# Optimization experiments

Measured on AMD Instinct MI355X. Metric: run time of the kernel, lower is better.

## Reference

```python
import jax, jax.numpy as jnp
import numpy as np

N_USER = 100000
N_ITEM = 100000
SUPP = 10000
B = 1024
L = 50
S = 256
H = 4
E = 64
HID = 64


def setup_inputs() -> dict:
    key = jax.random.key(0)
    ks = jax.random.split(key, 32)
    f32 = jnp.float32
    inp = {}
    # forward int args
    inp["x"] = jax.random.randint(ks[0], (B, 2), 0, N_USER)
    inp["src_his"] = jax.random.randint(ks[1], (B, L), 0, N_ITEM)
    inp["src_hl"] = jax.random.randint(ks[2], (B,), 0, L)
    inp["tgt_his"] = jax.random.randint(ks[3], (B, L), 0, N_ITEM)
    inp["tgt_hl"] = jax.random.randint(ks[4], (B,), 0, L)
    # precomputed neighbor sampling: [2 get_user_emb calls, H heads, B, S]
    inp["sample_idx"] = jax.random.randint(ks[5], (2, H, B, S), 0, SUPP)
    inp["supp_users"] = jax.random.randint(ks[6], (SUPP,), 0, N_USER)
    # embedding tables (xavier-ish small scale)
    inp["src_user_emb"] = jax.random.normal(ks[7], (N_USER, E), f32) * 0.1
    inp["src_item_emb"] = jax.random.normal(ks[8], (N_ITEM, E), f32) * 0.1
    inp["tgt_user_emb"] = jax.random.normal(ks[9], (N_USER, E), f32) * 0.1
    inp["tgt_item_emb"] = jax.random.normal(ks[10], (N_ITEM, E), f32) * 0.1
    # attention / aggregation weights, stored [in, out]
    s = 1.0 / np.sqrt(E)
    inp["W_att_w"] = jax.random.normal(ks[11], (E, E), f32) * s
    inp["W_att_b"] = jnp.full((E,), 0.1, f32)
    inp["W_agg_w"] = jax.random.normal(ks[12], (E, E), f32) * s
    # per-head GAT projections, batched over heads
    inp["Wq"] = jax.random.normal(ks[13], (H, E, E), f32) * s
    inp["Wk"] = jax.random.normal(ks[14], (H, E, E), f32) * s
    inp["Wv"] = jax.random.normal(ks[15], (H, E, E), f32) * s
    inp["W_out"] = jax.random.normal(ks[16], (H * E, E), f32) * (1.0 / np.sqrt(H * E))
    # scoring MLP
    inp["l1_w"] = jax.random.normal(ks[17], (2 * E, HID), f32) * (1.0 / np.sqrt(2 * E))
    inp["l1_b"] = jnp.full((HID,), 0.1, f32)
    inp["l2_w"] = jax.random.normal(ks[18], (HID, E), f32) * (1.0 / np.sqrt(HID))
    inp["l2_b"] = jnp.full((E,), 0.1, f32)
    inp["l3_w"] = jax.random.normal(ks[19], (E, 1), f32) * s
    inp["l3_b"] = jnp.full((1,), 0.1, f32)
    return inp


def reference(x, src_his, src_hl, tgt_his, tgt_hl, sample_idx, supp_users,
              src_user_emb, src_item_emb, tgt_user_emb, tgt_item_emb,
              W_att_w, W_att_b, W_agg_w, Wq, Wk, Wv, W_out,
              l1_w, l1_b, l2_w, l2_b, l3_w, l3_b):
    user_id = x[:, 0]
    item_id = x[:, 1]

    def user_fea_encode(his, hl, user_table):
        # NOTE: original always gathers from src_model.item_embedding (even for tgt)
        Lh = his.shape[1]
        valid = jnp.arange(Lh)[None, :] < hl[:, None]          # [B,L]
        hist = src_item_emb[his] * valid[..., None]             # [B,L,E], padded rows zeroed
        u = user_table[user_id]                                 # [B,E]
        keyt = jnp.tanh(hist @ W_att_w + W_att_b)               # [B,L,E]
        pad = hist.sum(-1) == 0                                 # [B,L]
        att = jnp.einsum('ble,be->bl', keyt, u)
        # faithful masked_softmax: masked scores set to 0 BEFORE exp (exp(0)=1 still contributes)
        att = jnp.where(pad, 0.0, att)
        e = jnp.exp(att)
        att = e / (jnp.sum(e, axis=1, keepdims=True) + 1e-12)
        out = jnp.einsum('bl,ble->be', att, hist)
        return out @ W_agg_w                                    # W_agg has no bias

    def get_user_emb(fea, idx):
        # idx: [H,B,S] indices into supp_users; all heads batched in one einsum chain
        neigh = tgt_user_emb[supp_users[idx]]                   # [H,B,S,E]
        q = jnp.einsum('be,heo->hbo', fea, Wq)                  # [H,B,O]
        k = jnp.einsum('hbse,heo->hbso', neigh, Wk)             # [H,B,S,O]
        attn = jax.nn.softmax(jnp.einsum('hbo,hbso->hbs', q, k), axis=-1)
        ctx = jnp.einsum('hbs,hbso->hbo', attn, k)              # weighted sum over neighbors
        g = jnp.einsum('hbo,hop->hbp', ctx, Wv)                 # [H,B,O]
        g = jnp.transpose(g, (1, 0, 2)).reshape(fea.shape[0], -1)  # concat heads -> [B,H*O]
        return g @ W_out

    user_src_fea = user_fea_encode(src_his, src_hl, src_user_emb)
    user_emb = get_user_emb(user_src_fea, sample_idx[0])
    item_emb = tgt_item_emb[item_id]
    user_tgt_fea = user_fea_encode(tgt_his, tgt_hl, tgt_user_emb)
    hybrid_tgt_emb = get_user_emb(user_tgt_fea, sample_idx[1])

    x_t = jnp.concatenate([hybrid_tgt_emb, item_emb], axis=1)
    x1_t = jnp.tanh(x_t @ l1_w + l1_b)
    x2_t = jnp.tanh(x1_t @ l2_w + l2_b)
    x3_t = (x2_t @ l3_w + l3_b).reshape(-1)

    output = jnp.sum(user_emb * item_emb, axis=1)
    out_emb_s = user_emb * item_emb
    # (output, output_t, out_emb_s, out_emb_t); train=False branch (sim/domain heads are None)
    return (output, x3_t, out_emb_s, x2_t)
```

## Files before the change

### kernel.cpp

```cpp
#include <hip/hip_runtime.h>

constexpr int B    = 1024;
constexpr int L    = 50;
constexpr int S    = 256;
constexpr int H    = 4;
constexpr int E    = 64;
constexpr int HID  = 64;
constexpr int SUPP = 10000;

__device__ __forceinline__ float lanebc(float v, int l) {
    return __int_as_float(__builtin_amdgcn_readlane(__float_as_int(v), l));
}

__global__ __launch_bounds__(256) void pre_kernel(
    const int* __restrict__ x,
    const int* __restrict__ src_his,
    const int* __restrict__ src_hl,
    const int* __restrict__ tgt_his,
    const int* __restrict__ tgt_hl,
    const float* __restrict__ item_emb,
    const float* __restrict__ src_user_emb,
    const float* __restrict__ tgt_user_emb,
    const int* __restrict__ supp_users,
    const float* __restrict__ W_att_w,
    const float* __restrict__ W_att_b,
    const float* __restrict__ W_agg_w,
    const float* __restrict__ Wq,
    const float* __restrict__ Wk,
    float* __restrict__ qout,
    float* __restrict__ K_supp)
{
    const int tid  = threadIdx.x;
    const int lane = tid & 63;
    const int wave = tid >> 6;

    if (blockIdx.y == 2) {
        const int h = wave;
        float wcol[E];
#pragma unroll
        for (int i = 0; i < E; i++) wcol[i] = Wk[h * E * E + i * E + lane];

#pragma unroll 2
        for (int j = blockIdx.x; j < SUPP; j += gridDim.x) {
            const int u = supp_users[j];
            const float ev = tgt_user_emb[(size_t)u * E + lane];
            float acc = 0.0f;
#pragma unroll
            for (int i = 0; i < E; i++) acc += lanebc(ev, i) * wcol[i];
            K_supp[((size_t)h * SUPP + j) * E + lane] = acc;
        }
        return;
    }

    __shared__ float sHist[L * E];
    __shared__ float sAtt[L];
    __shared__ float sPart[4][E];
    __shared__ float sOut[E];

    const int b    = blockIdx.x;
    const int call = blockIdx.y;

    const int* his = call ? tgt_his : src_his;
    const int* hl  = call ? tgt_hl  : src_hl;
    const float* user_table = call ? tgt_user_emb : src_user_emb;

    float wcol[E];
#pragma unroll
    for (int i = 0; i < E; i++) wcol[i] = W_att_w[i * E + lane];

    const int uid    = x[2 * b];
    const float uv   = user_table[(size_t)uid * E + lane];
    const float bias = W_att_b[lane];
    const int hlen   = hl[b];

    for (int l = wave; l < L; l += 4) {
        const int it = his[b * L + l];
        const float hv = (l < hlen) ? item_emb[(size_t)it * E + lane] : 0.0f;
        sHist[l * E + lane] = hv;
        float a = bias;
#pragma unroll
        for (int i = 0; i < E; i++) a += lanebc(hv, i) * wcol[i];
        float part = tanhf(a) * uv;
        float hsum = hv;
#pragma unroll
        for (int off = 32; off; off >>= 1) {
            part += __shfl_xor(part, off);
            hsum += __shfl_xor(hsum, off);
        }
        if (lane == 0) sAtt[l] = (hsum == 0.0f) ? 0.0f : part;
    }
    __syncthreads();

    if (wave == 0) {
        float v = (lane < L) ? expf(sAtt[lane]) : 0.0f;
        float s = v;
#pragma unroll
        for (int off = 32; off; off >>= 1) s += __shfl_xor(s, off);
        const float denom = s + 1e-12f;
        if (lane < L) sAtt[lane] = v / denom;
    }
    __syncthreads();

    float c = 0.0f;
    for (int l = wave; l < L; l += 4) c += sAtt[l] * sHist[l * E + lane];
    sPart[wave][lane] = c;
    __syncthreads();
    if (tid < E) sOut[tid] = sPart[0][tid] + sPart[1][tid] + sPart[2][tid] + sPart[3][tid];
    __syncthreads();

    float g = 0.0f;
#pragma unroll
    for (int k = 0; k < 16; k++) {
        const int i = wave * 16 + k;
        g += sOut[i] * W_agg_w[i * E + lane];
    }
    sPart[wave][lane] = g;
    __syncthreads();

    const float fval = sPart[0][lane] + sPart[1][lane] + sPart[2][lane] + sPart[3][lane];
    const float* Wqh = Wq + wave * E * E;
    float qacc = 0.0f;
#pragma unroll
    for (int i = 0; i < E; i++) qacc += lanebc(fval, i) * Wqh[i * E + lane];
    qout[(((call * H) + wave) * B + b) * E + lane] = qacc;
}

__global__ __launch_bounds__(256) void attn_kernel(
    const int* __restrict__ sample_idx,
    const float* __restrict__ K_supp,
    const float* __restrict__ qarr,
    const float* __restrict__ Wv,
    float* __restrict__ gout)
{
    __shared__ float sRed[8];
    __shared__ float sCtx[4][E];
    __shared__ float sC[E];
    __shared__ float sG[4][E];

    const int b    = blockIdx.x;
    const int h    = blockIdx.y;
    const int call = blockIdx.z;
    const int tid  = threadIdx.x;
    const int lane = tid & 63;
    const int wave = tid >> 6;
    const int u    = lane & 15;
    const int rsub = lane >> 4;
    const int s0   = wave * 64;

    const int* idx = sample_idx + (((call * H) + h) * B + b) * S;
    const float* Kh = K_supp + (size_t)h * SUPP * E;
    const float4 qu = *(const float4*)(qarr + ((size_t)(((call * H) + h) * B + b)) * E + 4 * u);

    float4 kreg[16];
    float mylogit = 0.0f;
#pragma unroll
    for (int i = 0; i < 16; i++) {
        const int j = idx[s0 + 4 * i + rsub];
        kreg[i] = *(const float4*)(Kh + (size_t)j * E + 4 * u);
        float part = kreg[i].x * qu.x + kreg[i].y * qu.y
                   + kreg[i].z * qu.z + kreg[i].w * qu.w;
#pragma unroll
        for (int off = 1; off < 16; off <<= 1) part += __shfl_xor(part, off);
        mylogit = (u == i) ? part : mylogit;
    }

    float m = mylogit;
#pragma unroll
    for (int off = 32; off; off >>= 1) m = fmaxf(m, __shfl_xor(m, off));
    if (lane == 0) sRed[wave] = m;
    __syncthreads();
    const float mx = fmaxf(fmaxf(sRed[0], sRed[1]), fmaxf(sRed[2], sRed[3]));
    const float ex = expf(mylogit - mx);
    float sm = ex;
#pragma unroll
    for (int off = 32; off; off >>= 1) sm += __shfl_xor(sm, off);
    if (lane == 0) sRed[4 + wave] = sm;
    __syncthreads();
    const float denom = sRed[4] + sRed[5] + sRed[6] + sRed[7];
    const float pval = ex / denom;

    float4 cacc = make_float4(0.0f, 0.0f, 0.0f, 0.0f);
#pragma unroll
    for (int i = 0; i < 16; i++) {
        const float p = __shfl(pval, (lane & 48) + i);
        cacc.x += p * kreg[i].x;
        cacc.y += p * kreg[i].y;
        cacc.z += p * kreg[i].z;
        cacc.w += p * kreg[i].w;
    }
#pragma unroll
    for (int off = 16; off <= 32; off <<= 1) {
        cacc.x += __shfl_xor(cacc.x, off);
        cacc.y += __shfl_xor(cacc.y, off);
        cacc.z += __shfl_xor(cacc.z, off);
        cacc.w += __shfl_xor(cacc.w, off);
    }
    if (lane < 16) *(float4*)(&sCtx[wave][u * 4]) = cacc;
    __syncthreads();
    if (wave == 0) {
        sC[lane] = sCtx[0][lane] + sCtx[1][lane] + sCtx[2][lane] + sCtx[3][lane];
    }
    __syncthreads();

    const float* Wvh = Wv + h * E * E;
    float g = 0.0f;
#pragma unroll
    for (int k = 0; k < 16; k++) {
        const int c = wave * 16 + k;
        g += sC[c] * Wvh[c * E + lane];
    }
    sG[wave][lane] = g;
    __syncthreads();
    if (wave == 0) {
        gout[((size_t)(call * B) + b) * (H * E) + h * E + lane] =
            sG[0][lane] + sG[1][lane] + sG[2][lane] + sG[3][lane];
    }
}

__global__ __launch_bounds__(256) void final_kernel(
    const int* __restrict__ x,
    const float* __restrict__ tgt_item_emb,
    const float* __restrict__ gsrc,
    const float* __restrict__ gtgt,
    const float* __restrict__ W_out,
    const float* __restrict__ l1_w,
    const float* __restrict__ l1_b,
    const float* __restrict__ l2_w,
    const float* __restrict__ l2_b,
    const float* __restrict__ l3_w,
    const float* __restrict__ l3_b,
    float* __restrict__ out)
{
    __shared__ float sPart[4][E];
    __shared__ float sHyb[E];
    __shared__ float sItem[E];
    __shared__ float sX1[HID];

    const int b    = blockIdx.x;
    const int tid  = threadIdx.x;
    const int lane = tid & 63;
    const int wave = tid >> 6;

    if (tid < E) {
        const int item = x[2 * b + 1];
        sItem[tid] = tgt_item_emb[(size_t)item * E + tid];
    }

    const float* grow = (wave < 2) ? (gsrc + (size_t)b * (H * E))
                                   : (gtgt + (size_t)b * (H * E));
    const int i0 = (wave & 1) * 128;
    float acc = 0.0f;
    for (int i = i0; i < i0 + 128; i++) {
        acc += grow[i] * W_out[i * E + lane];
    }
    sPart[wave][lane] = acc;
    __syncthreads();

    if (wave == 0) {
        const float ue = sPart[0][lane] + sPart[1][lane];
        const float prod = ue * sItem[lane];
        out[2 * B + b * E + lane] = prod;
        float s = prod;
#pragma unroll
        for (int off = 32; off; off >>= 1) s += __shfl_xor(s, off);
        if (lane == 0) out[b] = s;
    }
    if (wave == 1) {
        sHyb[lane] = sPart[2][lane] + sPart[3][lane];
    }
    __syncthreads();

    float a1 = 0.0f;
#pragma unroll
    for (int k = 0; k < 32; k++) {
        const int i = wave * 32 + k;
        const float v = (i < 64) ? sHyb[i] : sItem[i - 64];
        a1 += v * l1_w[i * HID + lane];
    }
    sPart[wave][lane] = a1;
    __syncthreads();

    if (wave == 0) {
        const float a = l1_b[lane] + sPart[0][lane] + sPart[1][lane]
                      + sPart[2][lane] + sPart[3][lane];
        sX1[lane] = tanhf(a);
    }
    __syncthreads();

    if (wave == 0) {
        float a = l2_b[lane];
#pragma unroll
        for (int i = 0; i < HID; i++) a += sX1[i] * l2_w[i * E + lane];
        const float x2 = tanhf(a);
        out[2 * B + B * E + b * E + lane] = x2;
        float p = x2 * l3_w[lane];
#pragma unroll
        for (int off = 32; off; off >>= 1) p += __shfl_xor(p, off);
        if (lane == 0) out[B + b] = p + l3_b[0];
    }
}

extern "C" void kernel_launch(void* const* d_in, const int* in_sizes, int n_in,
                              void* d_out, int out_size, void* d_ws, size_t ws_size,
                              hipStream_t stream) {
    const int*   x            = (const int*)d_in[0];
    const int*   src_his      = (const int*)d_in[1];
    const int*   src_hl       = (const int*)d_in[2];
    const int*   tgt_his      = (const int*)d_in[3];
    const int*   tgt_hl       = (const int*)d_in[4];
    const int*   sample_idx   = (const int*)d_in[5];
    const int*   supp_users   = (const int*)d_in[6];
    const float* src_user_emb = (const float*)d_in[7];
    const float* src_item_emb = (const float*)d_in[8];
    const float* tgt_user_emb = (const float*)d_in[9];
    const float* tgt_item_emb = (const float*)d_in[10];
    const float* W_att_w      = (const float*)d_in[11];
    const float* W_att_b      = (const float*)d_in[12];
    const float* W_agg_w      = (const float*)d_in[13];
    const float* Wq           = (const float*)d_in[14];
    const float* Wk           = (const float*)d_in[15];
    const float* Wv           = (const float*)d_in[16];
    const float* W_out        = (const float*)d_in[17];
    const float* l1_w         = (const float*)d_in[18];
    const float* l1_b         = (const float*)d_in[19];
    const float* l2_w         = (const float*)d_in[20];
    const float* l2_b         = (const float*)d_in[21];
    const float* l3_w         = (const float*)d_in[22];
    const float* l3_b         = (const float*)d_in[23];

    float* ws      = (float*)d_ws;
    float* qarr    = ws;
    float* K_supp  = qarr + 2 * H * B * E;
    float* garr    = K_supp + H * SUPP * E;
    float* out     = (float*)d_out;

    pre_kernel<<<dim3(B, 3), 256, 0, stream>>>(
        x, src_his, src_hl, tgt_his, tgt_hl, src_item_emb,
        src_user_emb, tgt_user_emb, supp_users,
        W_att_w, W_att_b, W_agg_w, Wq, Wk, qarr, K_supp);
    attn_kernel<<<dim3(B, H, 2), 256, 0, stream>>>(
        sample_idx, K_supp, qarr, Wv, garr);
    final_kernel<<<dim3(B), 256, 0, stream>>>(
        x, tgt_item_emb, garr, garr + B * H * E, W_out,
        l1_w, l1_b, l2_w, l2_b, l3_w, l3_b, out);
}
```

Before: 278.6 us.

## Split dot-product accumulators, prefetch history rows, and parallelize l2 across waves

Rewrites the serial dot-product reductions in all kernels to use four independent accumulators, which breaks the FMA dependency chains. The history loop in pre_kernel now software-prefetches the next item embedding row so the gather overlaps with compute. In final_kernel the l2 layer is split across all four waves with a shared-memory reduction, where before only wave 0 computed it. This adds a sync and changes the floating-point summation order slightly.

```diff
diff --git a/kernel.cpp b/kernel.cpp
--- a/kernel.cpp
+++ b/kernel.cpp
@@ -10,6 +10,18 @@
 
 __device__ __forceinline__ float lanebc(float v, int l) {
     return __int_as_float(__builtin_amdgcn_readlane(__float_as_int(v), l));
+}
+
+__device__ __forceinline__ float bcdot64(float v, const float* w) {
+    float a0 = 0.0f, a1 = 0.0f, a2 = 0.0f, a3 = 0.0f;
+#pragma unroll
+    for (int i = 0; i < E; i += 4) {
+        a0 += lanebc(v, i)     * w[i];
+        a1 += lanebc(v, i + 1) * w[i + 1];
+        a2 += lanebc(v, i + 2) * w[i + 2];
+        a3 += lanebc(v, i + 3) * w[i + 3];
+    }
+    return (a0 + a1) + (a2 + a3);
 }
 
 __global__ __launch_bounds__(256) void pre_kernel(
@@ -44,10 +56,7 @@
         for (int j = blockIdx.x; j < SUPP; j += gridDim.x) {
             const int u = supp_users[j];
             const float ev = tgt_user_emb[(size_t)u * E + lane];
-            float acc = 0.0f;
-#pragma unroll
-            for (int i = 0; i < E; i++) acc += lanebc(ev, i) * wcol[i];
-            K_supp[((size_t)h * SUPP + j) * E + lane] = acc;
+            K_supp[((size_t)h * SUPP + j) * E + lane] = bcdot64(ev, wcol);
         }
         return;
     }
@@ -73,21 +82,33 @@
     const float bias = W_att_b[lane];
     const int hlen   = hl[b];
 
-    for (int l = wave; l < L; l += 4) {
-        const int it = his[b * L + l];
-        const float hv = (l < hlen) ? item_emb[(size_t)it * E + lane] : 0.0f;
-        sHist[l * E + lane] = hv;
-        float a = bias;
-#pragma unroll
-        for (int i = 0; i < E; i++) a += lanebc(hv, i) * wcol[i];
-        float part = tanhf(a) * uv;
-        float hsum = hv;
-#pragma unroll
-        for (int off = 32; off; off >>= 1) {
-            part += __shfl_xor(part, off);
-            hsum += __shfl_xor(hsum, off);
-        }
-        if (lane == 0) sAtt[l] = (hsum == 0.0f) ? 0.0f : part;
+    {
+        int l = wave;
+        float hv = 0.0f;
+        if (l < L) {
+            const int it = his[b * L + l];
+            hv = (l < hlen) ? item_emb[(size_t)it * E + lane] : 0.0f;
+        }
+        while (l < L) {
+            const int lnext = l + 4;
+            float hv_next = 0.0f;
+            if (lnext < L) {
+                const int it = his[b * L + lnext];
+                hv_next = (lnext < hlen) ? item_emb[(size_t)it * E + lane] : 0.0f;
+            }
+            sHist[l * E + lane] = hv;
+            const float a = bias + bcdot64(hv, wcol);
+            float part = tanhf(a) * uv;
+            float hsum = hv;
+#pragma unroll
+            for (int off = 32; off; off >>= 1) {
+                part += __shfl_xor(part, off);
+                hsum += __shfl_xor(hsum, off);
+            }
+            if (lane == 0) sAtt[l] = (hsum == 0.0f) ? 0.0f : part;
+            hv = hv_next;
+            l  = lnext;
+        }
     }
     __syncthreads();
 
@@ -101,28 +122,41 @@
     }
     __syncthreads();
 
-    float c = 0.0f;
-    for (int l = wave; l < L; l += 4) c += sAtt[l] * sHist[l * E + lane];
-    sPart[wave][lane] = c;
+    {
+        float c0 = 0.0f, c1 = 0.0f;
+        for (int l = wave; l < L; l += 8) c0 += sAtt[l] * sHist[l * E + lane];
+        for (int l = wave + 4; l < L; l += 8) c1 += sAtt[l] * sHist[l * E + lane];
+        sPart[wave][lane] = c0 + c1;
+    }
     __syncthreads();
     if (tid < E) sOut[tid] = sPart[0][tid] + sPart[1][tid] + sPart[2][tid] + sPart[3][tid];
     __syncthreads();
 
-    float g = 0.0f;
-#pragma unroll
-    for (int k = 0; k < 16; k++) {
-        const int i = wave * 16 + k;
-        g += sOut[i] * W_agg_w[i * E + lane];
-    }
-    sPart[wave][lane] = g;
+    {
+        float g0 = 0.0f, g1 = 0.0f, g2 = 0.0f, g3 = 0.0f;
+#pragma unroll
+        for (int k = 0; k < 16; k += 4) {
+            const int i = wave * 16 + k;
+            g0 += sOut[i]     * W_agg_w[i * E + lane];
+            g1 += sOut[i + 1] * W_agg_w[(i + 1) * E + lane];
+            g2 += sOut[i + 2] * W_agg_w[(i + 2) * E + lane];
+            g3 += sOut[i + 3] * W_agg_w[(i + 3) * E + lane];
+        }
+        sPart[wave][lane] = (g0 + g1) + (g2 + g3);
+    }
     __syncthreads();
 
     const float fval = sPart[0][lane] + sPart[1][lane] + sPart[2][lane] + sPart[3][lane];
     const float* Wqh = Wq + wave * E * E;
-    float qacc = 0.0f;
-#pragma unroll
-    for (int i = 0; i < E; i++) qacc += lanebc(fval, i) * Wqh[i * E + lane];
-    qout[(((call * H) + wave) * B + b) * E + lane] = qacc;
+    float q0 = 0.0f, q1 = 0.0f, q2 = 0.0f, q3 = 0.0f;
+#pragma unroll
+    for (int i = 0; i < E; i += 4) {
+        q0 += lanebc(fval, i)     * Wqh[i * E + lane];
+        q1 += lanebc(fval, i + 1) * Wqh[(i + 1) * E + lane];
+        q2 += lanebc(fval, i + 2) * Wqh[(i + 2) * E + lane];
+        q3 += lanebc(fval, i + 3) * Wqh[(i + 3) * E + lane];
+    }
+    qout[(((call * H) + wave) * B + b) * E + lane] = (q0 + q1) + (q2 + q3);
 }
 
 __global__ __launch_bounds__(256) void attn_kernel(
@@ -203,13 +237,16 @@
     __syncthreads();
 
     const float* Wvh = Wv + h * E * E;
-    float g = 0.0f;
-#pragma unroll
-    for (int k = 0; k < 16; k++) {
+    float g0 = 0.0f, g1 = 0.0f, g2 = 0.0f, g3 = 0.0f;
+#pragma unroll
+    for (int k = 0; k < 16; k += 4) {
         const int c = wave * 16 + k;
-        g += sC[c] * Wvh[c * E + lane];
-    }
-    sG[wave][lane] = g;
+        g0 += sC[c]     * Wvh[c * E + lane];
+        g1 += sC[c + 1] * Wvh[(c + 1) * E + lane];
+        g2 += sC[c + 2] * Wvh[(c + 2) * E + lane];
+        g3 += sC[c + 3] * Wvh[(c + 3) * E + lane];
+    }
+    sG[wave][lane] = (g0 + g1) + (g2 + g3);
     __syncthreads();
     if (wave == 0) {
         gout[((size_t)(call * B) + b) * (H * E) + h * E + lane] =
@@ -249,11 +286,14 @@
     const float* grow = (wave < 2) ? (gsrc + (size_t)b * (H * E))
                                    : (gtgt + (size_t)b * (H * E));
     const int i0 = (wave & 1) * 128;
-    float acc = 0.0f;
-    for (int i = i0; i < i0 + 128; i++) {
-        acc += grow[i] * W_out[i * E + lane];
-    }
-    sPart[wave][lane] = acc;
+    float a0 = 0.0f, a1 = 0.0f, a2 = 0.0f, a3 = 0.0f;
+    for (int i = i0; i < i0 + 128; i += 4) {
+        a0 += grow[i]     * W_out[i * E + lane];
+        a1 += grow[i + 1] * W_out[(i + 1) * E + lane];
+        a2 += grow[i + 2] * W_out[(i + 2) * E + lane];
+        a3 += grow[i + 3] * W_out[(i + 3) * E + lane];
+    }
+    sPart[wave][lane] = (a0 + a1) + (a2 + a3);
     __syncthreads();
 
     if (wave == 0) {
@@ -270,14 +310,22 @@
     }
     __syncthreads();
 
-    float a1 = 0.0f;
-#pragma unroll
-    for (int k = 0; k < 32; k++) {
-        const int i = wave * 32 + k;
-        const float v = (i < 64) ? sHyb[i] : sItem[i - 64];
-        a1 += v * l1_w[i * HID + lane];
-    }
-    sPart[wave][lane] = a1;
+    {
+        float b0 = 0.0f, b1 = 0.0f, b2 = 0.0f, b3 = 0.0f;
+#pragma unroll
+        for (int k = 0; k < 32; k += 4) {
+            const int i = wave * 32 + k;
+            const float v0 = (i < 64)     ? sHyb[i]          : sItem[i - 64];
+            const float v1 = (i + 1 < 64) ? sHyb[i + 1]      : sItem[i + 1 - 64];
+            const float v2 = (i + 2 < 64) ? sHyb[i + 2]      : sItem[i + 2 - 64];
+            const float v3 = (i + 3 < 64) ? sHyb[i + 3]      : sItem[i + 3 - 64];
+            b0 += v0 * l1_w[i * HID + lane];
+            b1 += v1 * l1_w[(i + 1) * HID + lane];
+            b2 += v2 * l1_w[(i + 2) * HID + lane];
+            b3 += v3 * l1_w[(i + 3) * HID + lane];
+        }
+        sPart[wave][lane] = (b0 + b1) + (b2 + b3);
+    }
     __syncthreads();
 
     if (wave == 0) {
@@ -287,10 +335,23 @@
     }
     __syncthreads();
 
-    if (wave == 0) {
-        float a = l2_b[lane];
-#pragma unroll
-        for (int i = 0; i < HID; i++) a += sX1[i] * l2_w[i * E + lane];
+    {
+        float c0 = 0.0f, c1 = 0.0f, c2 = 0.0f, c3 = 0.0f;
+#pragma unroll
+        for (int k = 0; k < 16; k += 4) {
+            const int i = wave * 16 + k;
+            c0 += sX1[i]     * l2_w[i * E + lane];
+            c1 += sX1[i + 1] * l2_w[(i + 1) * E + lane];
+            c2 += sX1[i + 2] * l2_w[(i + 2) * E + lane];
+            c3 += sX1[i + 3] * l2_w[(i + 3) * E + lane];
+        }
+        sPart[wave][lane] = (c0 + c1) + (c2 + c3);
+    }
+    __syncthreads();
+
+    if (wave == 0) {
+        const float a = l2_b[lane] + sPart[0][lane] + sPart[1][lane]
+                      + sPart[2][lane] + sPart[3][lane];
         const float x2 = tanhf(a);
         out[2 * B + B * E + b * E + lane] = x2;
         float p = x2 * l3_w[lane];
```

New measurement: 290.1 us. +4.1%, slower.
